# Performance work log

Hardware: AMD Instinct MI355X
Metric: run time of the kernel (lower is better)

Reference implementation:

```python
import jax, jax.numpy as jnp
import numpy as np

L, D, H, V, T_MAX, DFF = 8, 1024, 16, 50257, 1024, 4096
HS = D // H
EPS = 1e-5


def setup_inputs() -> dict:
    key = jax.random.key(0)
    ks = jax.random.split(key, 20)
    s = 0.02
    inp = {
        "idx": jax.random.randint(ks[0], (4, 1024), 0, V),
        "wte": jax.random.normal(ks[1], (V, D), jnp.float32) * s,
        "wpe": jax.random.normal(ks[2], (T_MAX, D), jnp.float32) * s,
        "wq": jax.random.normal(ks[3], (L, D, D), jnp.float32) * s,
        "wk": jax.random.normal(ks[4], (L, D, D), jnp.float32) * s,
        "wv": jax.random.normal(ks[5], (L, D, D), jnp.float32) * s,
        "wo": jax.random.normal(ks[6], (L, D, D), jnp.float32) * s,
        "bo": jnp.zeros((L, D), jnp.float32),
        "ln1_w": jnp.ones((L, D), jnp.float32),
        "ln1_b": jnp.zeros((L, D), jnp.float32),
        "ln2_w": jnp.ones((L, D), jnp.float32),
        "ln2_b": jnp.zeros((L, D), jnp.float32),
        "w1": jax.random.normal(ks[7], (L, D, DFF), jnp.float32) * s,
        "b1": jnp.zeros((L, DFF), jnp.float32),
        "w2": jax.random.normal(ks[8], (L, DFF, D), jnp.float32) * s,
        "b2": jnp.zeros((L, D), jnp.float32),
        "lnf_w": jnp.ones((D,), jnp.float32),
        "lnf_b": jnp.zeros((D,), jnp.float32),
        "wlm": jax.random.normal(ks[9], (D, V), jnp.float32) * s,
        "blm": jnp.zeros((V,), jnp.float32),
    }
    return inp


def _ln(x, w, b):
    mu = jnp.mean(x, axis=-1, keepdims=True)
    var = jnp.mean(jnp.square(x - mu), axis=-1, keepdims=True)
    return (x - mu) * jax.lax.rsqrt(var + EPS) * w + b


def _gpt_forward(idx, wte, wpe, wq, wk, wv, wo, bo, ln1_w, ln1_b, ln2_w, ln2_b,
                 w1, b1, w2, b2, lnf_w, lnf_b, wlm, blm):
    B, T = idx.shape
    x = wte[idx] + wpe[:T]                       # [B,T,D]
    causal = jnp.tril(jnp.ones((T, T), bool))    # same as tril buffer
    scale = HS ** -0.5
    for i in range(L):
        h = _ln(x, ln1_w[i], ln1_b[i])
        q = (h @ wq[i]).reshape(B, T, H, HS)
        k = (h @ wk[i]).reshape(B, T, H, HS)
        v = (h @ wv[i]).reshape(B, T, H, HS)
        wei = jnp.einsum('bqhd,bkhd->bhqk', q, k) * scale
        wei = jnp.where(causal, wei, -jnp.inf)
        wei = jax.nn.softmax(wei, axis=-1)
        attn = jnp.einsum('bhqk,bkhd->bqhd', wei, v).reshape(B, T, D)
        x = x + attn @ wo[i] + bo[i]
        h2 = _ln(x, ln2_w[i], ln2_b[i])
        x = x + jax.nn.relu(h2 @ w1[i] + b1[i]) @ w2[i] + b2[i]
    x = _ln(x, lnf_w, lnf_b)
    return x @ wlm + blm                          # logits [B,T,V]


def reference(idx, wte, wpe, wq, wk, wv, wo, bo, ln1_w, ln1_b, ln2_w, ln2_b,
              w1, b1, w2, b2, lnf_w, lnf_b, wlm, blm):
    return _gpt_forward(idx, wte, wpe, wq, wk, wv, wo, bo, ln1_w, ln1_b,
                        ln2_w, ln2_b, w1, b1, w2, b2, lnf_w, lnf_b, wlm, blm)
```

## Files before the change

### kernel.cpp

```cpp
#include <hip/hip_runtime.h>
#include <cstdint>
#include <cstddef>

typedef __attribute__((ext_vector_type(4))) float f32x4;
typedef __attribute__((ext_vector_type(8))) short s16x8;
typedef __attribute__((ext_vector_type(4))) unsigned short u16x4;
typedef __attribute__((ext_vector_type(2))) unsigned short u16x2;

#define NLAYER 8
#define DM 1024
#define NTOK 4096
#define DFF2 4096
#define NV 50257
#define NVPAD 50432

__device__ __forceinline__ unsigned short f2bf(float f) {
  unsigned int u = __float_as_uint(f);
  u = u + 0x7fffu + ((u >> 16) & 1u);
  return (unsigned short)(u >> 16);
}

__device__ __forceinline__ void gload_lds16(const void* gp, void* lp) {
  const __attribute__((address_space(1))) unsigned int* g =
      reinterpret_cast<const __attribute__((address_space(1))) unsigned int*>(
          reinterpret_cast<uintptr_t>(gp));
  __attribute__((address_space(3))) unsigned int* l =
      reinterpret_cast<__attribute__((address_space(3))) unsigned int*>(
          (unsigned int)(uintptr_t)lp);
  __builtin_amdgcn_global_load_lds(g, l, 16, 0, 0);
}

__global__ void __launch_bounds__(256) convT_k(const float* __restrict__ in,
                                               unsigned short* __restrict__ out,
                                               int K, int N, size_t zStride) {
  __shared__ float tile[64][65];
  const int n0 = blockIdx.x * 64, k0 = blockIdx.y * 64;
  const float* inp = in + (size_t)blockIdx.z * K * N;
  unsigned short* outp = out + (size_t)blockIdx.z * zStride;
  const int tid = threadIdx.x;
#pragma unroll
  for (int p = 0; p < 16; ++p) {
    const int r = p * 4 + (tid >> 6);
    const int cc = tid & 63;
    const int gn = n0 + cc;
    tile[r][cc] = (gn < N) ? inp[(size_t)(k0 + r) * N + gn] : 0.f;
  }
  __syncthreads();
#pragma unroll
  for (int p = 0; p < 8; ++p) {
    const int lin = p * 256 + tid;
    const int rn = lin >> 5;
    const int c2 = (lin & 31) * 2;
    u16x2 o;
    o[0] = f2bf(tile[c2][rn]);
    o[1] = f2bf(tile[c2 + 1][rn]);
    *(u16x2*)&outp[(size_t)(n0 + rn) * K + k0 + c2] = o;
  }
}

__global__ void __launch_bounds__(256) embed_k(const int* __restrict__ idx,
                                               const float* __restrict__ wte,
                                               const float* __restrict__ wpe,
                                               float* __restrict__ X) {
  const int tok = blockIdx.x;
  const int t = tok & 1023;
  const int id = idx[tok];
  const int c = threadIdx.x * 4;
  f32x4 a = *(const f32x4*)&wte[(size_t)id * DM + c];
  f32x4 p = *(const f32x4*)&wpe[(size_t)t * DM + c];
  a = a + p;
  *(f32x4*)&X[(size_t)tok * DM + c] = a;
}

__global__ void __launch_bounds__(256) ln_k(const float* __restrict__ X,
                                            const float* __restrict__ W,
                                            const float* __restrict__ Bp,
                                            unsigned short* __restrict__ O) {
  const int row = blockIdx.x, tid = threadIdx.x;
  const size_t base = (size_t)row * DM;
  f32x4 v = *(const f32x4*)&X[base + tid * 4];
  float s = v[0] + v[1] + v[2] + v[3];
  float q = v[0] * v[0] + v[1] * v[1] + v[2] * v[2] + v[3] * v[3];
#pragma unroll
  for (int m = 1; m < 64; m <<= 1) {
    s += __shfl_xor(s, m);
    q += __shfl_xor(q, m);
  }
  __shared__ float ps[4], pq[4];
  const int wv = tid >> 6;
  if ((tid & 63) == 0) { ps[wv] = s; pq[wv] = q; }
  __syncthreads();
  s = ps[0] + ps[1] + ps[2] + ps[3];
  q = pq[0] + pq[1] + pq[2] + pq[3];
  const float mu = s * (1.f / DM);
  const float var = q * (1.f / DM) - mu * mu;
  const float rstd = rsqrtf(var + 1e-5f);
  f32x4 w = *(const f32x4*)&W[tid * 4];
  f32x4 bb = *(const f32x4*)&Bp[tid * 4];
  u16x4 o;
#pragma unroll
  for (int j = 0; j < 4; ++j) o[j] = f2bf((v[j] - mu) * rstd * w[j] + bb[j]);
  *(u16x4*)&O[base + tid * 4] = o;
}

__global__ void __launch_bounds__(256) reduce2ln_k(
    float* __restrict__ X, const float* __restrict__ bias,
    const float* __restrict__ P0, const float* __restrict__ P1,
    const float* __restrict__ W, const float* __restrict__ Bp,
    unsigned short* __restrict__ O) {
  const int row = blockIdx.x, tid = threadIdx.x;
  const size_t base = (size_t)row * DM;
  const size_t i = base + tid * 4;
  f32x4 v = *(f32x4*)&X[i];
  {
    f32x4 b = *(const f32x4*)&bias[tid * 4];
    f32x4 a = *(const f32x4*)&P0[i];
    f32x4 c = *(const f32x4*)&P1[i];
    v = v + b + a + c;
    *(f32x4*)&X[i] = v;
  }
  float s = v[0] + v[1] + v[2] + v[3];
  float q = v[0] * v[0] + v[1] * v[1] + v[2] * v[2] + v[3] * v[3];
#pragma unroll
  for (int m = 1; m < 64; m <<= 1) {
    s += __shfl_xor(s, m);
    q += __shfl_xor(q, m);
  }
  __shared__ float ps[4], pq[4];
  const int wv = tid >> 6;
  if ((tid & 63) == 0) { ps[wv] = s; pq[wv] = q; }
  __syncthreads();
  s = ps[0] + ps[1] + ps[2] + ps[3];
  q = pq[0] + pq[1] + pq[2] + pq[3];
  const float mu = s * (1.f / DM);
  const float var = q * (1.f / DM) - mu * mu;
  const float rstd = rsqrtf(var + 1e-5f);
  f32x4 w = *(const f32x4*)&W[tid * 4];
  f32x4 bb = *(const f32x4*)&Bp[tid * 4];
  u16x4 o;
#pragma unroll
  for (int j = 0; j < 4; ++j) o[j] = f2bf((v[j] - mu) * rstd * w[j] + bb[j]);
  *(u16x4*)&O[base + tid * 4] = o;
}

__global__ void __launch_bounds__(256) gemm_k(
    const unsigned short* __restrict__ A, const unsigned short* __restrict__ Bt,
    const float* __restrict__ bias, float* __restrict__ outF,
    unsigned short* __restrict__ outB, unsigned short* __restrict__ vt,
    int M, int N, int K, int lda, int ldc) {
  __shared__ __align__(16) unsigned short lA[128 * 64];
  __shared__ __align__(16) unsigned short lB[128 * 64];
  const int tid = threadIdx.x;
  const int wv = tid >> 6, lane = tid & 63;
  const int row0 = blockIdx.y * 128, col0 = blockIdx.x * 128;
  const int wr = wv >> 1, wc = wv & 1;

  const int z = blockIdx.z;
  A += (size_t)z * K;
  Bt += (size_t)z * K;
  if (gridDim.z > 1) outF += (size_t)z * M * ldc;

  f32x4 acc[4][4] = {};

  const int sRow = tid >> 3;
  const int sColSw = ((tid & 7) * 8) ^ ((sRow & 7) * 8);
  const unsigned short* gA = A + (size_t)(row0 + sRow) * lda + sColSw;
  const unsigned short* gB = Bt + (size_t)(col0 + sRow) * lda + sColSw;
  unsigned short* lAd = lA + tid * 8;
  unsigned short* lBd = lB + tid * 8;
  const size_t step32 = (size_t)32 * lda;

  const int rbase = lane & 15;
  const int kHi = (lane >> 4) * 8;
  const int kSw = (lane & 7) * 8;

  for (int kt = 0; kt < K; kt += 64) {
#pragma unroll
    for (int i = 0; i < 4; ++i) {
      gload_lds16(gA + kt + i * step32, lAd + i * 2048);
      gload_lds16(gB + kt + i * step32, lBd + i * 2048);
    }
    __syncthreads();
    s16x8 af[2][4], bfr[2][4];
#pragma unroll
    for (int kk = 0; kk < 2; ++kk) {
      const int kph = (kk * 32 + kHi) ^ kSw;
#pragma unroll
      for (int m = 0; m < 4; ++m)
        af[kk][m] = *(const s16x8*)&lA[(wr * 64 + m * 16 + rbase) * 64 + kph];
#pragma unroll
      for (int n = 0; n < 4; ++n)
        bfr[kk][n] = *(const s16x8*)&lB[(wc * 64 + n * 16 + rbase) * 64 + kph];
    }
#pragma unroll
    for (int kk = 0; kk < 2; ++kk)
#pragma unroll
      for (int m = 0; m < 4; ++m)
#pragma unroll
        for (int n = 0; n < 4; ++n)
          acc[m][n] = __builtin_amdgcn_mfma_f32_16x16x32_bf16(
              af[kk][m], bfr[kk][n], acc[m][n], 0, 0, 0);
    __syncthreads();
  }

  const int baseRow = row0 + wr * 64 + ((lane >> 4) * 4);
  const int baseCol = col0 + wc * 64 + (lane & 15);
#pragma unroll
  for (int m = 0; m < 4; ++m) {
#pragma unroll
    for (int n = 0; n < 4; ++n) {
      const int colc = baseCol + n * 16;
      if (colc < N) {
        const int rowc0 = baseRow + m * 16;
        if (vt && colc >= 2048) {
          const int f = colc - 2048;
          const int b = rowc0 >> 10, t0 = rowc0 & 1023;
          u16x4 o;
#pragma unroll
          for (int r = 0; r < 4; ++r) o[r] = f2bf(acc[m][n][r]);
          *(u16x4*)&vt[((size_t)((b << 4) + (f >> 6)) * 64 + (f & 63)) * 1024 + t0] = o;
        } else {
          const float bv = bias ? bias[colc] : 0.f;
#pragma unroll
          for (int r = 0; r < 4; ++r) {
            float v = acc[m][n][r] + bv;
            if (outF) outF[(size_t)(rowc0 + r) * ldc + colc] = v;
            if (outB) outB[(size_t)(rowc0 + r) * ldc + colc] = f2bf(v);
          }
        }
      }
    }
  }
}

__global__ void __launch_bounds__(512, 2) gemm256_k(
    const unsigned short* __restrict__ A, const unsigned short* __restrict__ Bt,
    const float* __restrict__ bias, float* __restrict__ outF,
    unsigned short* __restrict__ outB, int M, int N, int K, int lda, int ldc,
    int relu) {
  __shared__ __align__(16) unsigned short lA[2][256 * 64];
  __shared__ __align__(16) unsigned short lB[2][256 * 64];
  const int tid = threadIdx.x;
  const int wv = tid >> 6, lane = tid & 63;
  const int row0 = blockIdx.y * 256, col0 = blockIdx.x * 256;
  const int wr = wv >> 2, wc = wv & 3;

  f32x4 acc[8][4] = {};

  const int sRow = tid >> 3;
  const int sColSw = ((tid & 7) * 8) ^ ((sRow & 7) * 8);
  const unsigned short* gA = A + (size_t)(row0 + sRow) * lda + sColSw;
  const unsigned short* gB = Bt + (size_t)(col0 + sRow) * lda + sColSw;
  const size_t step64 = (size_t)64 * lda;
  const int ldsBase = wv * 512;

  const int rbase = lane & 15;
  const int g8 = (lane >> 4) * 8;
  const int kSw = (lane & 7) * 8;

  const int nt = K >> 6;
#pragma unroll
  for (int i = 0; i < 4; ++i) {
    gload_lds16(gA + i * step64, &lA[0][i * 4096 + ldsBase]);
    gload_lds16(gB + i * step64, &lB[0][i * 4096 + ldsBase]);
  }
  for (int t = 0; t < nt; ++t) {
    const int cur = t & 1, nxt = cur ^ 1;
    const int ktn = (t + 1) << 6;
    __syncthreads();
    const unsigned short* lAp = &lA[cur][0];
    const unsigned short* lBp = &lB[cur][0];
#pragma unroll
    for (int q = 0; q < 4; ++q) {
      if (t + 1 < nt) {
        gload_lds16(gA + ktn + q * step64, &lA[nxt][q * 4096 + ldsBase]);
        gload_lds16(gB + ktn + q * step64, &lB[nxt][q * 4096 + ldsBase]);
      }
      const int qm = q & 1, qn = q >> 1;
      s16x8 af[4][2], bfr[2][2];
#pragma unroll
      for (int ks = 0; ks < 2; ++ks) {
        const int kph = (ks * 32 + g8) ^ kSw;
#pragma unroll
        for (int m = 0; m < 4; ++m)
          af[m][ks] = *(const s16x8*)
              &lAp[(wr * 128 + qm * 64 + m * 16 + rbase) * 64 + kph];
#pragma unroll
        for (int n = 0; n < 2; ++n)
          bfr[n][ks] = *(const s16x8*)
              &lBp[(wc * 64 + qn * 32 + n * 16 + rbase) * 64 + kph];
      }
      __builtin_amdgcn_s_setprio(1);
#pragma unroll
      for (int m = 0; m < 4; ++m)
#pragma unroll
        for (int n = 0; n < 2; ++n)
#pragma unroll
          for (int ks = 0; ks < 2; ++ks)
            acc[qm * 4 + m][qn * 2 + n] = __builtin_amdgcn_mfma_f32_16x16x32_bf16(
                af[m][ks], bfr[n][ks], acc[qm * 4 + m][qn * 2 + n], 0, 0, 0);
      __builtin_amdgcn_s_setprio(0);
    }
  }

  const int baseRow = row0 + wr * 128 + ((lane >> 4) * 4);
  const int baseCol = col0 + wc * 64 + (lane & 15);
#pragma unroll
  for (int m = 0; m < 8; ++m) {
#pragma unroll
    for (int n = 0; n < 4; ++n) {
      const int colc = baseCol + n * 16;
      if (colc < N) {
        const float bv = bias ? bias[colc] : 0.f;
        const int rowc0 = baseRow + m * 16;
#pragma unroll
        for (int r = 0; r < 4; ++r) {
          float v = acc[m][n][r] + bv;
          if (relu) v = fmaxf(v, 0.f);
          if (outF) outF[(size_t)(rowc0 + r) * ldc + colc] = v;
          if (outB) outB[(size_t)(rowc0 + r) * ldc + colc] = f2bf(v);
        }
      }
    }
  }
}

__global__ void __launch_bounds__(256) attn_k(const unsigned short* __restrict__ Q,
                                              const unsigned short* __restrict__ Kb,
                                              const unsigned short* __restrict__ Vt,
                                              unsigned short* __restrict__ O,
                                              int ldq) {
  const int qt = blockIdx.x;
  const int bh = blockIdx.y;
  const int b = bh >> 4, h = bh & 15;
  const int tid = threadIdx.x, wv = tid >> 6, lane = tid & 63;
  const int g = lane >> 4, c = lane & 15;
  __shared__ __align__(16) unsigned short lP[4][16 * 64];
  const int qw0 = qt * 64 + wv * 16;
  s16x8 qf0, qf1;
  {
    const size_t qoff = ((size_t)(b * 1024 + qw0 + c)) * ldq + h * 64 + g * 8;
    qf0 = *(const s16x8*)&Q[qoff];
    qf1 = *(const s16x8*)&Q[qoff + 32];
  }
  f32x4 acc[4] = {};
  float mrun[4], lrun[4];
#pragma unroll
  for (int r = 0; r < 4; ++r) { mrun[r] = -1e30f; lrun[r] = 0.f; }

  for (int kt = 0; kt <= qt; ++kt) {
    f32x4 s[4] = {};
#pragma unroll
    for (int n = 0; n < 4; ++n) {
      const size_t koff = ((size_t)(b * 1024 + kt * 64 + n * 16 + c)) * ldq + h * 64 + g * 8;
      s16x8 k0 = *(const s16x8*)&Kb[koff];
      s16x8 k1 = *(const s16x8*)&Kb[koff + 32];
      s[n] = __builtin_amdgcn_mfma_f32_16x16x32_bf16(qf0, k0, s[n], 0, 0, 0);
      s[n] = __builtin_amdgcn_mfma_f32_16x16x32_bf16(qf1, k1, s[n], 0, 0, 0);
    }
    float p[4][4], mx[4] = {-1e30f, -1e30f, -1e30f, -1e30f};
#pragma unroll
    for (int n = 0; n < 4; ++n)
#pragma unroll
      for (int r = 0; r < 4; ++r) {
        const int qrow = qw0 + g * 4 + r;
        const int key = kt * 64 + n * 16 + c;
        float v = s[n][r] * 0.125f;
        if (key > qrow) v = -1e30f;
        p[n][r] = v;
        mx[r] = fmaxf(mx[r], v);
      }
#pragma unroll
    for (int r = 0; r < 4; ++r)
#pragma unroll
      for (int m = 1; m <= 8; m <<= 1) mx[r] = fmaxf(mx[r], __shfl_xor(mx[r], m));
    float al[4], rs[4];
#pragma unroll
    for (int r = 0; r < 4; ++r) {
      const float mn = fmaxf(mrun[r], mx[r]);
      al[r] = __expf(mrun[r] - mn);
      mrun[r] = mn;
      rs[r] = 0.f;
    }
#pragma unroll
    for (int n = 0; n < 4; ++n)
#pragma unroll
      for (int r = 0; r < 4; ++r) {
        const float e = __expf(p[n][r] - mrun[r]);
        p[n][r] = e;
        rs[r] += e;
      }
#pragma unroll
    for (int r = 0; r < 4; ++r) {
#pragma unroll
      for (int m = 1; m <= 8; m <<= 1) rs[r] += __shfl_xor(rs[r], m);
      lrun[r] = lrun[r] * al[r] + rs[r];
    }
#pragma unroll
    for (int n = 0; n < 4; ++n)
#pragma unroll
      for (int r = 0; r < 4; ++r) acc[n][r] *= al[r];
    __syncthreads();
#pragma unroll
    for (int n = 0; n < 4; ++n)
#pragma unroll
      for (int r = 0; r < 4; ++r)
        lP[wv][(g * 4 + r) * 64 + n * 16 + c] = f2bf(p[n][r]);
    __syncthreads();
    s16x8 pa0 = *(const s16x8*)&lP[wv][c * 64 + g * 8];
    s16x8 pa1 = *(const s16x8*)&lP[wv][c * 64 + 32 + g * 8];
#pragma unroll
    for (int n = 0; n < 4; ++n) {
      const size_t voff = ((size_t)(bh * 64 + n * 16 + c)) * 1024 + kt * 64 + g * 8;
      s16x8 v0 = *(const s16x8*)&Vt[voff];
      s16x8 v1 = *(const s16x8*)&Vt[voff + 32];
      acc[n] = __builtin_amdgcn_mfma_f32_16x16x32_bf16(pa0, v0, acc[n], 0, 0, 0);
      acc[n] = __builtin_amdgcn_mfma_f32_16x16x32_bf16(pa1, v1, acc[n], 0, 0, 0);
    }
  }
#pragma unroll
  for (int n = 0; n < 4; ++n)
#pragma unroll
    for (int r = 0; r < 4; ++r) {
      const size_t row = (size_t)(b * 1024 + qw0 + g * 4 + r);
      O[row * DM + h * 64 + n * 16 + c] = f2bf(acc[n][r] / lrun[r]);
    }
}

extern "C" void kernel_launch(void* const* d_in, const int* in_sizes, int n_in,
                              void* d_out, int out_size, void* d_ws, size_t ws_size,
                              hipStream_t stream) {
  const int* idx = (const int*)d_in[0];
  const float* wte = (const float*)d_in[1];
  const float* wpe = (const float*)d_in[2];
  const float* wq = (const float*)d_in[3];
  const float* wk = (const float*)d_in[4];
  const float* wv = (const float*)d_in[5];
  const float* wo = (const float*)d_in[6];
  const float* bo = (const float*)d_in[7];
  const float* ln1w = (const float*)d_in[8];
  const float* ln1b = (const float*)d_in[9];
  const float* ln2w = (const float*)d_in[10];
  const float* ln2b = (const float*)d_in[11];
  const float* w1 = (const float*)d_in[12];
  const float* b1 = (const float*)d_in[13];
  const float* w2 = (const float*)d_in[14];
  const float* b2 = (const float*)d_in[15];
  const float* lnfw = (const float*)d_in[16];
  const float* lnfb = (const float*)d_in[17];
  const float* wlm = (const float*)d_in[18];
  const float* blm = (const float*)d_in[19];
  float* out = (float*)d_out;

  char* ws = (char*)d_ws;
  size_t off = 0;
  auto alloc = [&](size_t bytes) -> void* {
    void* p = ws + off;
    off += (bytes + 255) & ~(size_t)255;
    return p;
  };
  unsigned short* wqkvT = (unsigned short*)alloc((size_t)NLAYER * 3072 * DM * 2);
  unsigned short* woT = (unsigned short*)alloc((size_t)NLAYER * DM * DM * 2);
  unsigned short* w1T = (unsigned short*)alloc((size_t)NLAYER * DM * DFF2 * 2);
  unsigned short* w2T = (unsigned short*)alloc((size_t)NLAYER * DM * DFF2 * 2);
  unsigned short* wlmT = w1T;
  float* X = (float*)alloc((size_t)NTOK * DM * 4);
  unsigned short* Hb = (unsigned short*)alloc((size_t)NTOK * DM * 2);
  char* uni = (char*)alloc((size_t)32 * 1024 * 1024);
  unsigned short* QKVb = (unsigned short*)uni;
  unsigned short* Ab = (unsigned short*)(uni + (size_t)24 * 1024 * 1024);
  float* P0 = (float*)uni;
  float* P1 = (float*)(uni + (size_t)16 * 1024 * 1024);
  unsigned short* VtB = (unsigned short*)alloc((size_t)NTOK * DM * 2);
  unsigned short* Mid = (unsigned short*)alloc((size_t)NTOK * DFF2 * 2);
  float* MidF = (float*)Mid;

  const size_t qkvStride = (size_t)3072 * DM;
  convT_k<<<dim3(16, 16, 8), 256, 0, stream>>>(wq, wqkvT, DM, DM, qkvStride);
  convT_k<<<dim3(16, 16, 8), 256, 0, stream>>>(wk, wqkvT + (size_t)1024 * DM, DM, DM, qkvStride);
  convT_k<<<dim3(16, 16, 8), 256, 0, stream>>>(wv, wqkvT + (size_t)2048 * DM, DM, DM, qkvStride);
  convT_k<<<dim3(16, 16, 8), 256, 0, stream>>>(wo, woT, DM, DM, (size_t)DM * DM);
  convT_k<<<dim3(64, 16, 8), 256, 0, stream>>>(w1, w1T, DM, DFF2, (size_t)DM * DFF2);
  convT_k<<<dim3(16, 64, 8), 256, 0, stream>>>(w2, w2T, DFF2, DM, (size_t)DM * DFF2);

  embed_k<<<dim3(NTOK), 256, 0, stream>>>(idx, wte, wpe, X);
  ln_k<<<dim3(NTOK), 256, 0, stream>>>(X, ln1w, ln1b, Hb);

  for (int i = 0; i < NLAYER; ++i) {
    const size_t wOff = (size_t)i * DM * DM;
    const size_t fOff = (size_t)i * DM * DFF2;
    gemm_k<<<dim3(24, 32), 256, 0, stream>>>(Hb, wqkvT + i * qkvStride, nullptr,
                                             nullptr, QKVb, VtB, NTOK, 3072, DM,
                                             DM, 3072);
    attn_k<<<dim3(16, 64), 256, 0, stream>>>(QKVb, QKVb + 1024, VtB, Ab, 3072);
    gemm_k<<<dim3(8, 32, 2), 256, 0, stream>>>(Ab, woT + wOff, nullptr, MidF,
                                               nullptr, nullptr, NTOK, DM,
                                               DM / 2, DM, DM);
    reduce2ln_k<<<dim3(NTOK), 256, 0, stream>>>(X, bo + i * DM, MidF,
                                                MidF + (size_t)NTOK * DM,
                                                ln2w + i * DM, ln2b + i * DM, Hb);
    gemm256_k<<<dim3(16, 16), 512, 0, stream>>>(Hb, w1T + fOff, b1 + i * DFF2,
                                                nullptr, Mid, NTOK, DFF2, DM,
                                                DM, DFF2, 1);
    gemm_k<<<dim3(8, 32, 2), 256, 0, stream>>>(Mid, w2T + fOff, nullptr, P0,
                                               nullptr, nullptr, NTOK, DM,
                                               DFF2 / 2, DFF2, DM);
    const float* nw = (i < NLAYER - 1) ? ln1w + (i + 1) * DM : lnfw;
    const float* nb = (i < NLAYER - 1) ? ln1b + (i + 1) * DM : lnfb;
    reduce2ln_k<<<dim3(NTOK), 256, 0, stream>>>(X, b2 + i * DM, P0, P1, nw, nb, Hb);
  }

  convT_k<<<dim3(788, 16, 1), 256, 0, stream>>>(wlm, wlmT, DM, NV, 0);
  gemm256_k<<<dim3(197, 16), 512, 0, stream>>>(Hb, wlmT, blm, out, nullptr, NTOK,
                                               NV, DM, DM, NV, 0);
}
```

Measured before the change: 3.414 ms.

## Add 4-stage pipelined 256x256 GEMM and use it for QKV, FFN1 and LM head

Replaces the double-buffered 256x256 GEMM with a new kernel that streams K in 32-wide slices through a 4-deep LDS ring. It uses direct global-to-LDS loads, explicit vmcnt waits and a single barrier per step, with an XOR swizzle for the 32-wide rows. The QKV projection moves from the 128x128 kernel to this one, and the V-transpose epilogue moves with it. The aim is to hide global-load latency better and cut barrier overhead. The risk is lower occupancy: the QKV GEMM now runs only 192 blocks.

New measurement: 3.331 ms. 2.4% less time.

```diff
diff --git a/kernel.cpp b/kernel.cpp
--- a/kernel.cpp
+++ b/kernel.cpp
@@ -146,8 +146,7 @@
 __global__ void __launch_bounds__(256) gemm_k(
     const unsigned short* __restrict__ A, const unsigned short* __restrict__ Bt,
     const float* __restrict__ bias, float* __restrict__ outF,
-    unsigned short* __restrict__ outB, unsigned short* __restrict__ vt,
-    int M, int N, int K, int lda, int ldc) {
+    unsigned short* __restrict__ outB, int M, int N, int K, int lda, int ldc) {
   __shared__ __align__(16) unsigned short lA[128 * 64];
   __shared__ __align__(16) unsigned short lB[128 * 64];
   const int tid = threadIdx.x;
@@ -207,6 +206,103 @@
   const int baseCol = col0 + wc * 64 + (lane & 15);
 #pragma unroll
   for (int m = 0; m < 4; ++m) {
+#pragma unroll
+    for (int n = 0; n < 4; ++n) {
+      const int colc = baseCol + n * 16;
+      if (colc < N) {
+        const float bv = bias ? bias[colc] : 0.f;
+        const int rowc0 = baseRow + m * 16;
+#pragma unroll
+        for (int r = 0; r < 4; ++r) {
+          float v = acc[m][n][r] + bv;
+          if (outF) outF[(size_t)(rowc0 + r) * ldc + colc] = v;
+          if (outB) outB[(size_t)(rowc0 + r) * ldc + colc] = f2bf(v);
+        }
+      }
+    }
+  }
+}
+
+__global__ void __launch_bounds__(512, 2) gemm256p_k(
+    const unsigned short* __restrict__ A, const unsigned short* __restrict__ Bt,
+    const float* __restrict__ bias, float* __restrict__ outF,
+    unsigned short* __restrict__ outB, unsigned short* __restrict__ vt,
+    int M, int N, int K, int lda, int ldc, int relu) {
+  __shared__ __align__(16) unsigned short lds[4][2][8192];
+  const int tid = threadIdx.x;
+  const int wv = tid >> 6, lane = tid & 63;
+  const int row0 = blockIdx.y * 256, col0 = blockIdx.x * 256;
+  const int wr = wv >> 2, wc = wv & 3;
+
+  f32x4 acc[8][4] = {};
+
+  const int sRow = tid >> 2;
+  const int sCol = ((tid & 3) ^ ((tid >> 3) & 3)) * 8;
+  const unsigned short* gA = A + (size_t)(row0 + sRow) * lda + sCol;
+  const unsigned short* gB = Bt + (size_t)(col0 + sRow) * lda + sCol;
+  const size_t step128 = (size_t)128 * lda;
+
+  const int rbase = lane & 15;
+  const int grp = ((lane >> 4) ^ ((lane >> 1) & 3)) * 8;
+
+  const int nt = K >> 5;
+
+#define STG(t, x, g)                                              \
+  {                                                               \
+    unsigned short* d = &lds[(t) & 3][x][tid * 8];                \
+    gload_lds16((g) + (size_t)(t) * 32, d);                       \
+    gload_lds16((g) + (size_t)(t) * 32 + step128, d + 4096);      \
+  }
+
+  STG(0, 0, gA); STG(0, 1, gB);
+  STG(1, 0, gA); STG(1, 1, gB);
+  STG(2, 0, gA); STG(2, 1, gB);
+  asm volatile("s_waitcnt vmcnt(8)" ::: "memory");
+  __builtin_amdgcn_s_barrier();
+
+  for (int t = 0; t < nt; ++t) {
+    const unsigned short* la = &lds[t & 3][0][0];
+    const unsigned short* lb = &lds[t & 3][1][0];
+    s16x8 bf[4], af[4];
+#pragma unroll
+    for (int n = 0; n < 4; ++n)
+      bf[n] = *(const s16x8*)&lb[(wc * 64 + n * 16 + rbase) * 32 + grp];
+#pragma unroll
+    for (int m = 0; m < 4; ++m)
+      af[m] = *(const s16x8*)&la[(wr * 128 + m * 16 + rbase) * 32 + grp];
+    if (t + 3 < nt) STG(t + 3, 0, gA);
+    __builtin_amdgcn_s_setprio(1);
+#pragma unroll
+    for (int m = 0; m < 4; ++m)
+#pragma unroll
+      for (int n = 0; n < 4; ++n)
+        acc[m][n] = __builtin_amdgcn_mfma_f32_16x16x32_bf16(af[m], bf[n],
+                                                            acc[m][n], 0, 0, 0);
+    __builtin_amdgcn_s_setprio(0);
+#pragma unroll
+    for (int m = 0; m < 4; ++m)
+      af[m] = *(const s16x8*)&la[(wr * 128 + 64 + m * 16 + rbase) * 32 + grp];
+    if (t + 3 < nt) STG(t + 3, 1, gB);
+    __builtin_amdgcn_s_setprio(1);
+#pragma unroll
+    for (int m = 0; m < 4; ++m)
+#pragma unroll
+      for (int n = 0; n < 4; ++n)
+        acc[4 + m][n] = __builtin_amdgcn_mfma_f32_16x16x32_bf16(
+            af[m], bf[n], acc[4 + m][n], 0, 0, 0);
+    __builtin_amdgcn_s_setprio(0);
+    if (t < nt - 4)
+      asm volatile("s_waitcnt vmcnt(8)" ::: "memory");
+    else if (t == nt - 4)
+      asm volatile("s_waitcnt vmcnt(0)" ::: "memory");
+    __builtin_amdgcn_s_barrier();
+  }
+#undef STG
+
+  const int baseRow = row0 + wr * 128 + ((lane >> 4) * 4);
+  const int baseCol = col0 + wc * 64 + (lane & 15);
+#pragma unroll
+  for (int m = 0; m < 8; ++m) {
 #pragma unroll
     for (int n = 0; n < 4; ++n) {
       const int colc = baseCol + n * 16;
@@ -224,101 +320,10 @@
 #pragma unroll
           for (int r = 0; r < 4; ++r) {
             float v = acc[m][n][r] + bv;
+            if (relu) v = fmaxf(v, 0.f);
             if (outF) outF[(size_t)(rowc0 + r) * ldc + colc] = v;
             if (outB) outB[(size_t)(rowc0 + r) * ldc + colc] = f2bf(v);
           }
-        }
-      }
-    }
-  }
-}
-
-__global__ void __launch_bounds__(512, 2) gemm256_k(
-    const unsigned short* __restrict__ A, const unsigned short* __restrict__ Bt,
-    const float* __restrict__ bias, float* __restrict__ outF,
-    unsigned short* __restrict__ outB, int M, int N, int K, int lda, int ldc,
-    int relu) {
-  __shared__ __align__(16) unsigned short lA[2][256 * 64];
-  __shared__ __align__(16) unsigned short lB[2][256 * 64];
-  const int tid = threadIdx.x;
-  const int wv = tid >> 6, lane = tid & 63;
-  const int row0 = blockIdx.y * 256, col0 = blockIdx.x * 256;
-  const int wr = wv >> 2, wc = wv & 3;
-
-  f32x4 acc[8][4] = {};
-
-  const int sRow = tid >> 3;
-  const int sColSw = ((tid & 7) * 8) ^ ((sRow & 7) * 8);
-  const unsigned short* gA = A + (size_t)(row0 + sRow) * lda + sColSw;
-  const unsigned short* gB = Bt + (size_t)(col0 + sRow) * lda + sColSw;
-  const size_t step64 = (size_t)64 * lda;
-  const int ldsBase = wv * 512;
-
-  const int rbase = lane & 15;
-  const int g8 = (lane >> 4) * 8;
-  const int kSw = (lane & 7) * 8;
-
-  const int nt = K >> 6;
-#pragma unroll
-  for (int i = 0; i < 4; ++i) {
-    gload_lds16(gA + i * step64, &lA[0][i * 4096 + ldsBase]);
-    gload_lds16(gB + i * step64, &lB[0][i * 4096 + ldsBase]);
-  }
-  for (int t = 0; t < nt; ++t) {
-    const int cur = t & 1, nxt = cur ^ 1;
-    const int ktn = (t + 1) << 6;
-    __syncthreads();
-    const unsigned short* lAp = &lA[cur][0];
-    const unsigned short* lBp = &lB[cur][0];
-#pragma unroll
-    for (int q = 0; q < 4; ++q) {
-      if (t + 1 < nt) {
-        gload_lds16(gA + ktn + q * step64, &lA[nxt][q * 4096 + ldsBase]);
-        gload_lds16(gB + ktn + q * step64, &lB[nxt][q * 4096 + ldsBase]);
-      }
-      const int qm = q & 1, qn = q >> 1;
-      s16x8 af[4][2], bfr[2][2];
-#pragma unroll
-      for (int ks = 0; ks < 2; ++ks) {
-        const int kph = (ks * 32 + g8) ^ kSw;
-#pragma unroll
-        for (int m = 0; m < 4; ++m)
-          af[m][ks] = *(const s16x8*)
-              &lAp[(wr * 128 + qm * 64 + m * 16 + rbase) * 64 + kph];
-#pragma unroll
-        for (int n = 0; n < 2; ++n)
-          bfr[n][ks] = *(const s16x8*)
-              &lBp[(wc * 64 + qn * 32 + n * 16 + rbase) * 64 + kph];
-      }
-      __builtin_amdgcn_s_setprio(1);
-#pragma unroll
-      for (int m = 0; m < 4; ++m)
-#pragma unroll
-        for (int n = 0; n < 2; ++n)
-#pragma unroll
-          for (int ks = 0; ks < 2; ++ks)
-            acc[qm * 4 + m][qn * 2 + n] = __builtin_amdgcn_mfma_f32_16x16x32_bf16(
-                af[m][ks], bfr[n][ks], acc[qm * 4 + m][qn * 2 + n], 0, 0, 0);
-      __builtin_amdgcn_s_setprio(0);
-    }
-  }
-
-  const int baseRow = row0 + wr * 128 + ((lane >> 4) * 4);
-  const int baseCol = col0 + wc * 64 + (lane & 15);
-#pragma unroll
-  for (int m = 0; m < 8; ++m) {
-#pragma unroll
-    for (int n = 0; n < 4; ++n) {
-      const int colc = baseCol + n * 16;
-      if (colc < N) {
-        const float bv = bias ? bias[colc] : 0.f;
-        const int rowc0 = baseRow + m * 16;
-#pragma unroll
-        for (int r = 0; r < 4; ++r) {
-          float v = acc[m][n][r] + bv;
-          if (relu) v = fmaxf(v, 0.f);
-          if (outF) outF[(size_t)(rowc0 + r) * ldc + colc] = v;
-          if (outB) outB[(size_t)(rowc0 + r) * ldc + colc] = f2bf(v);
         }
       }
     }
@@ -489,28 +494,27 @@
   for (int i = 0; i < NLAYER; ++i) {
     const size_t wOff = (size_t)i * DM * DM;
     const size_t fOff = (size_t)i * DM * DFF2;
-    gemm_k<<<dim3(24, 32), 256, 0, stream>>>(Hb, wqkvT + i * qkvStride, nullptr,
-                                             nullptr, QKVb, VtB, NTOK, 3072, DM,
-                                             DM, 3072);
+    gemm256p_k<<<dim3(12, 16), 512, 0, stream>>>(Hb, wqkvT + i * qkvStride,
+                                                 nullptr, nullptr, QKVb, VtB,
+                                                 NTOK, 3072, DM, DM, 3072, 0);
     attn_k<<<dim3(16, 64), 256, 0, stream>>>(QKVb, QKVb + 1024, VtB, Ab, 3072);
     gemm_k<<<dim3(8, 32, 2), 256, 0, stream>>>(Ab, woT + wOff, nullptr, MidF,
-                                               nullptr, nullptr, NTOK, DM,
-                                               DM / 2, DM, DM);
+                                               nullptr, NTOK, DM, DM / 2, DM, DM);
     reduce2ln_k<<<dim3(NTOK), 256, 0, stream>>>(X, bo + i * DM, MidF,
                                                 MidF + (size_t)NTOK * DM,
                                                 ln2w + i * DM, ln2b + i * DM, Hb);
-    gemm256_k<<<dim3(16, 16), 512, 0, stream>>>(Hb, w1T + fOff, b1 + i * DFF2,
-                                                nullptr, Mid, NTOK, DFF2, DM,
-                                                DM, DFF2, 1);
+    gemm256p_k<<<dim3(16, 16), 512, 0, stream>>>(Hb, w1T + fOff, b1 + i * DFF2,
+                                                 nullptr, Mid, nullptr, NTOK,
+                                                 DFF2, DM, DM, DFF2, 1);
     gemm_k<<<dim3(8, 32, 2), 256, 0, stream>>>(Mid, w2T + fOff, nullptr, P0,
-                                               nullptr, nullptr, NTOK, DM,
-                                               DFF2 / 2, DFF2, DM);
+                                               nullptr, NTOK, DM, DFF2 / 2,
+                                               DFF2, DM);
     const float* nw = (i < NLAYER - 1) ? ln1w + (i + 1) * DM : lnfw;
     const float* nb = (i < NLAYER - 1) ? ln1b + (i + 1) * DM : lnfb;
     reduce2ln_k<<<dim3(NTOK), 256, 0, stream>>>(X, b2 + i * DM, P0, P1, nw, nb, Hb);
   }
 
   convT_k<<<dim3(788, 16, 1), 256, 0, stream>>>(wlm, wlmT, DM, NV, 0);
-  gemm256_k<<<dim3(197, 16), 512, 0, stream>>>(Hb, wlmT, blm, out, nullptr, NTOK,
-                                               NV, DM, DM, NV, 0);
-}
+  gemm256p_k<<<dim3(197, 16), 512, 0, stream>>>(Hb, wlmT, blm, out, nullptr,
+                                                nullptr, NTOK, NV, DM, DM, NV, 0);
+}
```

## Unify GEMMs into a 256x128 triple-buffered pipelined kernel with nontemporal logits

Applied to the files above, without the earlier changes.

Replaces the 128x128 single-buffered GEMM and the 256x256 double-buffered GEMM with one 512-thread kernel. It uses a 256x128 tile, a three-stage LDS ring with split staging, explicit vmcnt/lgkmcnt waits, barriers and MFMA priority hints. All layer GEMMs and the LM head now go through it, with ReLU fused and an optional nontemporal store used for the large logits output. The aim is to overlap global loads with MFMA work and to cut sync stalls. In exchange, the FFN and LM-head GEMMs use smaller tiles and so reload more data, and the large LDS footprint limits the kernel to one block per CU.

After: 3.422 ms. Within noise of the previous version (+0.2%).

```diff
diff --git a/kernel.cpp b/kernel.cpp
--- a/kernel.cpp
+++ b/kernel.cpp
@@ -143,16 +143,16 @@
   *(u16x4*)&O[base + tid * 4] = o;
 }
 
-__global__ void __launch_bounds__(256) gemm_k(
+__global__ void __launch_bounds__(512, 1) gemm3_k(
     const unsigned short* __restrict__ A, const unsigned short* __restrict__ Bt,
     const float* __restrict__ bias, float* __restrict__ outF,
     unsigned short* __restrict__ outB, unsigned short* __restrict__ vt,
-    int M, int N, int K, int lda, int ldc) {
-  __shared__ __align__(16) unsigned short lA[128 * 64];
-  __shared__ __align__(16) unsigned short lB[128 * 64];
+    int M, int N, int K, int lda, int ldc, int relu, int ntStore) {
+  __shared__ __align__(16) unsigned short lA[3][256 * 64];
+  __shared__ __align__(16) unsigned short lB[3][128 * 64];
   const int tid = threadIdx.x;
   const int wv = tid >> 6, lane = tid & 63;
-  const int row0 = blockIdx.y * 128, col0 = blockIdx.x * 128;
+  const int row0 = blockIdx.y * 256, col0 = blockIdx.x * 128;
   const int wr = wv >> 1, wc = wv & 1;
 
   const int z = blockIdx.z;
@@ -162,49 +162,90 @@
 
   f32x4 acc[4][4] = {};
 
-  const int sRow = tid >> 3;
-  const int sColSw = ((tid & 7) * 8) ^ ((sRow & 7) * 8);
-  const unsigned short* gA = A + (size_t)(row0 + sRow) * lda + sColSw;
-  const unsigned short* gB = Bt + (size_t)(col0 + sRow) * lda + sColSw;
-  unsigned short* lAd = lA + tid * 8;
-  unsigned short* lBd = lB + tid * 8;
-  const size_t step32 = (size_t)32 * lda;
+  const int sColSw = (((tid & 7) ^ ((tid >> 3) & 7))) * 8;
+  const unsigned short* gA = A + (size_t)(row0 + (tid >> 3)) * lda + sColSw;
+  const unsigned short* gB = Bt + (size_t)(col0 + (tid >> 3)) * lda + sColSw;
+  const size_t step64 = (size_t)64 * lda;
 
   const int rbase = lane & 15;
-  const int kHi = (lane >> 4) * 8;
   const int kSw = (lane & 7) * 8;
-
-  for (int kt = 0; kt < K; kt += 64) {
-#pragma unroll
-    for (int i = 0; i < 4; ++i) {
-      gload_lds16(gA + kt + i * step32, lAd + i * 2048);
-      gload_lds16(gB + kt + i * step32, lBd + i * 2048);
-    }
-    __syncthreads();
-    s16x8 af[2][4], bfr[2][4];
-#pragma unroll
-    for (int kk = 0; kk < 2; ++kk) {
-      const int kph = (kk * 32 + kHi) ^ kSw;
+  const int g8 = (lane >> 4) * 8;
+
+  const int nt = K >> 6;
+
+#define STGA(t, l) \
+  gload_lds16(gA + (size_t)(t) * 64 + (l) * step64, &lA[(t) % 3][(l) * 4096 + tid * 8])
+#define STGB(t, l) \
+  gload_lds16(gB + (size_t)(t) * 64 + (l) * step64, &lB[(t) % 3][(l) * 4096 + tid * 8])
+
+  STGA(0, 0); STGA(0, 1); STGA(0, 2); STGA(0, 3); STGB(0, 0); STGB(0, 1);
+  STGA(1, 0); STGA(1, 1); STGA(1, 2); STGA(1, 3); STGB(1, 0); STGB(1, 1);
+  asm volatile("s_waitcnt vmcnt(6)" ::: "memory");
+  __builtin_amdgcn_s_barrier();
+
+  for (int t = 0; t < nt; ++t) {
+    const unsigned short* la = &lA[t % 3][0];
+    const unsigned short* lb = &lB[t % 3][0];
+    const bool stg = (t + 2 < nt);
+    s16x8 af[4][2], bf[2][2];
+#pragma unroll
+    for (int ks = 0; ks < 2; ++ks) {
+      const int kph = (ks * 32 + g8) ^ kSw;
 #pragma unroll
       for (int m = 0; m < 4; ++m)
-        af[kk][m] = *(const s16x8*)&lA[(wr * 64 + m * 16 + rbase) * 64 + kph];
-#pragma unroll
-      for (int n = 0; n < 4; ++n)
-        bfr[kk][n] = *(const s16x8*)&lB[(wc * 64 + n * 16 + rbase) * 64 + kph];
-    }
-#pragma unroll
-    for (int kk = 0; kk < 2; ++kk)
-#pragma unroll
-      for (int m = 0; m < 4; ++m)
-#pragma unroll
-        for (int n = 0; n < 4; ++n)
+        af[m][ks] = *(const s16x8*)&la[(wr * 64 + m * 16 + rbase) * 64 + kph];
+#pragma unroll
+      for (int n = 0; n < 2; ++n)
+        bf[n][ks] = *(const s16x8*)&lb[(wc * 64 + n * 16 + rbase) * 64 + kph];
+    }
+    if (stg) { STGA(t + 2, 0); STGA(t + 2, 1); STGA(t + 2, 2); }
+    __builtin_amdgcn_s_barrier();
+    asm volatile("s_waitcnt lgkmcnt(0)" ::: "memory");
+    __builtin_amdgcn_s_setprio(1);
+#pragma unroll
+    for (int m = 0; m < 4; ++m)
+#pragma unroll
+      for (int n = 0; n < 2; ++n)
+#pragma unroll
+        for (int ks = 0; ks < 2; ++ks)
           acc[m][n] = __builtin_amdgcn_mfma_f32_16x16x32_bf16(
-              af[kk][m], bfr[kk][n], acc[m][n], 0, 0, 0);
-    __syncthreads();
-  }
+              af[m][ks], bf[n][ks], acc[m][n], 0, 0, 0);
+    __builtin_amdgcn_s_setprio(0);
+    __builtin_amdgcn_s_barrier();
+#pragma unroll
+    for (int ks = 0; ks < 2; ++ks) {
+      const int kph = (ks * 32 + g8) ^ kSw;
+#pragma unroll
+      for (int n = 0; n < 2; ++n)
+        bf[n][ks] =
+            *(const s16x8*)&lb[(wc * 64 + 32 + n * 16 + rbase) * 64 + kph];
+    }
+    if (stg) { STGA(t + 2, 3); STGB(t + 2, 0); STGB(t + 2, 1); }
+    __builtin_amdgcn_s_barrier();
+    asm volatile("s_waitcnt lgkmcnt(0)" ::: "memory");
+    __builtin_amdgcn_s_setprio(1);
+#pragma unroll
+    for (int m = 0; m < 4; ++m)
+#pragma unroll
+      for (int n = 0; n < 2; ++n)
+#pragma unroll
+        for (int ks = 0; ks < 2; ++ks)
+          acc[m][2 + n] = __builtin_amdgcn_mfma_f32_16x16x32_bf16(
+              af[m][ks], bf[n][ks], acc[m][2 + n], 0, 0, 0);
+    __builtin_amdgcn_s_setprio(0);
+    if (t + 1 < nt) {
+      if (stg)
+        asm volatile("s_waitcnt vmcnt(6)" ::: "memory");
+      else
+        asm volatile("s_waitcnt vmcnt(0)" ::: "memory");
+    }
+    __builtin_amdgcn_s_barrier();
+  }
+#undef STGA
+#undef STGB
 
   const int baseRow = row0 + wr * 64 + ((lane >> 4) * 4);
-  const int baseCol = col0 + wc * 64 + (lane & 15);
+  const int baseCol = col0 + wc * 64 + rbase;
 #pragma unroll
   for (int m = 0; m < 4; ++m) {
 #pragma unroll
@@ -224,101 +265,15 @@
 #pragma unroll
           for (int r = 0; r < 4; ++r) {
             float v = acc[m][n][r] + bv;
-            if (outF) outF[(size_t)(rowc0 + r) * ldc + colc] = v;
+            if (relu) v = fmaxf(v, 0.f);
+            if (outF) {
+              if (ntStore)
+                __builtin_nontemporal_store(v, &outF[(size_t)(rowc0 + r) * ldc + colc]);
+              else
+                outF[(size_t)(rowc0 + r) * ldc + colc] = v;
+            }
             if (outB) outB[(size_t)(rowc0 + r) * ldc + colc] = f2bf(v);
           }
-        }
-      }
-    }
-  }
-}
-
-__global__ void __launch_bounds__(512, 2) gemm256_k(
-    const unsigned short* __restrict__ A, const unsigned short* __restrict__ Bt,
-    const float* __restrict__ bias, float* __restrict__ outF,
-    unsigned short* __restrict__ outB, int M, int N, int K, int lda, int ldc,
-    int relu) {
-  __shared__ __align__(16) unsigned short lA[2][256 * 64];
-  __shared__ __align__(16) unsigned short lB[2][256 * 64];
-  const int tid = threadIdx.x;
-  const int wv = tid >> 6, lane = tid & 63;
-  const int row0 = blockIdx.y * 256, col0 = blockIdx.x * 256;
-  const int wr = wv >> 2, wc = wv & 3;
-
-  f32x4 acc[8][4] = {};
-
-  const int sRow = tid >> 3;
-  const int sColSw = ((tid & 7) * 8) ^ ((sRow & 7) * 8);
-  const unsigned short* gA = A + (size_t)(row0 + sRow) * lda + sColSw;
-  const unsigned short* gB = Bt + (size_t)(col0 + sRow) * lda + sColSw;
-  const size_t step64 = (size_t)64 * lda;
-  const int ldsBase = wv * 512;
-
-  const int rbase = lane & 15;
-  const int g8 = (lane >> 4) * 8;
-  const int kSw = (lane & 7) * 8;
-
-  const int nt = K >> 6;
-#pragma unroll
-  for (int i = 0; i < 4; ++i) {
-    gload_lds16(gA + i * step64, &lA[0][i * 4096 + ldsBase]);
-    gload_lds16(gB + i * step64, &lB[0][i * 4096 + ldsBase]);
-  }
-  for (int t = 0; t < nt; ++t) {
-    const int cur = t & 1, nxt = cur ^ 1;
-    const int ktn = (t + 1) << 6;
-    __syncthreads();
-    const unsigned short* lAp = &lA[cur][0];
-    const unsigned short* lBp = &lB[cur][0];
-#pragma unroll
-    for (int q = 0; q < 4; ++q) {
-      if (t + 1 < nt) {
-        gload_lds16(gA + ktn + q * step64, &lA[nxt][q * 4096 + ldsBase]);
-        gload_lds16(gB + ktn + q * step64, &lB[nxt][q * 4096 + ldsBase]);
-      }
-      const int qm = q & 1, qn = q >> 1;
-      s16x8 af[4][2], bfr[2][2];
-#pragma unroll
-      for (int ks = 0; ks < 2; ++ks) {
-        const int kph = (ks * 32 + g8) ^ kSw;
-#pragma unroll
-        for (int m = 0; m < 4; ++m)
-          af[m][ks] = *(const s16x8*)
-              &lAp[(wr * 128 + qm * 64 + m * 16 + rbase) * 64 + kph];
-#pragma unroll
-        for (int n = 0; n < 2; ++n)
-          bfr[n][ks] = *(const s16x8*)
-              &lBp[(wc * 64 + qn * 32 + n * 16 + rbase) * 64 + kph];
-      }
-      __builtin_amdgcn_s_setprio(1);
-#pragma unroll
-      for (int m = 0; m < 4; ++m)
-#pragma unroll
-        for (int n = 0; n < 2; ++n)
-#pragma unroll
-          for (int ks = 0; ks < 2; ++ks)
-            acc[qm * 4 + m][qn * 2 + n] = __builtin_amdgcn_mfma_f32_16x16x32_bf16(
-                af[m][ks], bfr[n][ks], acc[qm * 4 + m][qn * 2 + n], 0, 0, 0);
-      __builtin_amdgcn_s_setprio(0);
-    }
-  }
-
-  const int baseRow = row0 + wr * 128 + ((lane >> 4) * 4);
-  const int baseCol = col0 + wc * 64 + (lane & 15);
-#pragma unroll
-  for (int m = 0; m < 8; ++m) {
-#pragma unroll
-    for (int n = 0; n < 4; ++n) {
-      const int colc = baseCol + n * 16;
-      if (colc < N) {
-        const float bv = bias ? bias[colc] : 0.f;
-        const int rowc0 = baseRow + m * 16;
-#pragma unroll
-        for (int r = 0; r < 4; ++r) {
-          float v = acc[m][n][r] + bv;
-          if (relu) v = fmaxf(v, 0.f);
-          if (outF) outF[(size_t)(rowc0 + r) * ldc + colc] = v;
-          if (outB) outB[(size_t)(rowc0 + r) * ldc + colc] = f2bf(v);
         }
       }
     }
@@ -489,28 +444,28 @@
   for (int i = 0; i < NLAYER; ++i) {
     const size_t wOff = (size_t)i * DM * DM;
     const size_t fOff = (size_t)i * DM * DFF2;
-    gemm_k<<<dim3(24, 32), 256, 0, stream>>>(Hb, wqkvT + i * qkvStride, nullptr,
-                                             nullptr, QKVb, VtB, NTOK, 3072, DM,
-                                             DM, 3072);
+    gemm3_k<<<dim3(24, 16), 512, 0, stream>>>(Hb, wqkvT + i * qkvStride, nullptr,
+                                              nullptr, QKVb, VtB, NTOK, 3072, DM,
+                                              DM, 3072, 0, 0);
     attn_k<<<dim3(16, 64), 256, 0, stream>>>(QKVb, QKVb + 1024, VtB, Ab, 3072);
-    gemm_k<<<dim3(8, 32, 2), 256, 0, stream>>>(Ab, woT + wOff, nullptr, MidF,
-                                               nullptr, nullptr, NTOK, DM,
-                                               DM / 2, DM, DM);
+    gemm3_k<<<dim3(8, 16, 2), 512, 0, stream>>>(Ab, woT + wOff, nullptr, MidF,
+                                                nullptr, nullptr, NTOK, DM,
+                                                DM / 2, DM, DM, 0, 0);
     reduce2ln_k<<<dim3(NTOK), 256, 0, stream>>>(X, bo + i * DM, MidF,
                                                 MidF + (size_t)NTOK * DM,
                                                 ln2w + i * DM, ln2b + i * DM, Hb);
-    gemm256_k<<<dim3(16, 16), 512, 0, stream>>>(Hb, w1T + fOff, b1 + i * DFF2,
-                                                nullptr, Mid, NTOK, DFF2, DM,
-                                                DM, DFF2, 1);
-    gemm_k<<<dim3(8, 32, 2), 256, 0, stream>>>(Mid, w2T + fOff, nullptr, P0,
-                                               nullptr, nullptr, NTOK, DM,
-                                               DFF2 / 2, DFF2, DM);
+    gemm3_k<<<dim3(32, 16), 512, 0, stream>>>(Hb, w1T + fOff, b1 + i * DFF2,
+                                              nullptr, Mid, nullptr, NTOK, DFF2,
+                                              DM, DM, DFF2, 1, 0);
+    gemm3_k<<<dim3(8, 16, 2), 512, 0, stream>>>(Mid, w2T + fOff, nullptr, P0,
+                                                nullptr, nullptr, NTOK, DM,
+                                                DFF2 / 2, DFF2, DM, 0, 0);
     const float* nw = (i < NLAYER - 1) ? ln1w + (i + 1) * DM : lnfw;
     const float* nb = (i < NLAYER - 1) ? ln1b + (i + 1) * DM : lnfb;
     reduce2ln_k<<<dim3(NTOK), 256, 0, stream>>>(X, b2 + i * DM, P0, P1, nw, nb, Hb);
   }
 
   convT_k<<<dim3(788, 16, 1), 256, 0, stream>>>(wlm, wlmT, DM, NV, 0);
-  gemm256_k<<<dim3(197, 16), 512, 0, stream>>>(Hb, wlmT, blm, out, nullptr, NTOK,
-                                               NV, DM, DM, NV, 0);
-}
+  gemm3_k<<<dim3(394, 16), 512, 0, stream>>>(Hb, wlmT, blm, out, nullptr, nullptr,
+                                             NTOK, NV, DM, DM, NV, 0, 1);
+}
```
